# Optimization experiments

Hardware: AMD Instinct MI355X
Metric: run time of the kernel (lower is better)

The kernel has to match this reference:

```python
import jax, jax.numpy as jnp
import numpy as np

EMB_DIM = 512
LATENT_DIM = 64
D = EMB_DIM + LATENT_DIM  # 576, kernel input per side
H1, H2 = 512, 256         # MLPKernel hidden widths
B, N, M = 2, 1024, 256


def setup_inputs() -> dict:
    key = jax.random.key(0)
    ks = jax.random.split(key, 10)
    def w(k, shape, fan_in):
        return (jax.random.normal(k, shape, dtype=jnp.float32) / np.sqrt(fan_in)).astype(jnp.float32)
    return {
        "Phi_A": jax.random.normal(ks[0], (B, N, D), dtype=jnp.float32),
        "Phi_B": jax.random.normal(ks[1], (B, M, D), dtype=jnp.float32),
        # MLPKernel params: layer1 acts on concat([a,b]) (2D -> H1); split into A/B halves
        "W1a": w(ks[2], (D, H1), 2 * D),
        "W1b": w(ks[3], (D, H1), 2 * D),
        "b1": jnp.zeros((H1,), dtype=jnp.float32),
        "W2": w(ks[4], (H1, H2), H1),
        "b2": jnp.zeros((H2,), dtype=jnp.float32),
        "W3": w(ks[5], (H2, 1), H2),
        "b3": jnp.zeros((1,), dtype=jnp.float32),
    }


def reference(Phi_A, Phi_B, W1a, W1b, b1, W2, b2, W3, b3):
    # Pairwise MLP kernel: for every (n, m), MLP(concat(Phi_A[b,n], Phi_B[b,m])).
    # First layer on concat == a@W1a + b@W1b; project each side once, then broadcast-add.
    a_proj = jnp.einsum("bnd,dh->bnh", Phi_A, W1a)          # (B, N, H1)
    b_proj = jnp.einsum("bmd,dh->bmh", Phi_B, W1b)          # (B, M, H1)
    h1 = jax.nn.relu(a_proj[:, :, None, :] + b_proj[:, None, :, :] + b1)  # (B, N, M, H1)
    h2 = jax.nn.relu(jnp.einsum("bnmh,hk->bnmk", h1, W2) + b2)            # (B, N, M, H2)
    dro = jnp.einsum("bnmk,ko->bnmo", h2, W3)[..., 0] + b3[0]             # (B, N, M)
    return dro
```

## Files before the change

kernel.cpp:

```cpp
#include <hip/hip_runtime.h>

typedef float  f4  __attribute__((ext_vector_type(4)));
typedef __bf16 bf8 __attribute__((ext_vector_type(8)));

constexpr int B_ = 2, N_ = 1024, M_ = 256, D_ = 576, H1_ = 512, H2_ = 256;

__device__ __forceinline__ void gload_lds16(const void* g, void* l) {
    __builtin_amdgcn_global_load_lds((const __attribute__((address_space(1))) void*)g,
                                     (__attribute__((address_space(3))) void*)l, 16, 0, 0);
}

__global__ __launch_bounds__(256) void k_prep(
    const float* __restrict__ PhiA, const float* __restrict__ PhiB,
    const float* __restrict__ W1a, const float* __restrict__ W1b, const float* __restrict__ W2,
    __bf16* __restrict__ phiAb, __bf16* __restrict__ phiBb,
    __bf16* __restrict__ w1aT, __bf16* __restrict__ w1bT, __bf16* __restrict__ w2T) {
    __shared__ float tl[32][33];
    int bid = blockIdx.x;
    if (bid < 704) {
        const float* src; __bf16* dst; int R, C, t0;
        if (bid < 288)      { src = W1a; dst = w1aT; R = D_;  C = H1_; t0 = bid; }
        else if (bid < 576) { src = W1b; dst = w1bT; R = D_;  C = H1_; t0 = bid - 288; }
        else                { src = W2;  dst = w2T;  R = H1_; C = H2_; t0 = bid - 576; }
        const int tilesC = C / 32;
        const int r0 = (t0 / tilesC) * 32, c0 = (t0 % tilesC) * 32;
        const int tx = threadIdx.x & 31, ty = threadIdx.x >> 5;
        #pragma unroll
        for (int i = 0; i < 4; ++i)
            tl[ty + i * 8][tx] = src[(size_t)(r0 + ty + i * 8) * C + c0 + tx];
        __syncthreads();
        #pragma unroll
        for (int i = 0; i < 4; ++i)
            dst[(size_t)(c0 + ty + i * 8) * R + r0 + tx] = (__bf16)tl[tx][ty + i * 8];
    } else {
        int i = (bid - 704) * 2048 + threadIdx.x * 8;
        const float* s; __bf16* d;
        if (bid < 1280) { s = PhiA; d = phiAb; }
        else            { s = PhiB; d = phiBb; i -= 1179648; }
        f4 v0 = *(const f4*)(s + i), v1 = *(const f4*)(s + i + 4);
        bf8 o;
        #pragma unroll
        for (int j = 0; j < 4; ++j) { o[j] = (__bf16)v0[j]; o[4 + j] = (__bf16)v1[j]; }
        *(bf8*)(d + i) = o;
    }
}

__global__ __launch_bounds__(256, 2) void k_proj(
    const __bf16* __restrict__ phiAb, const __bf16* __restrict__ phiBb,
    const __bf16* __restrict__ w1aT, const __bf16* __restrict__ w1bT,
    const float* __restrict__ b1, float* __restrict__ aproj, __bf16* __restrict__ bprojh) {
    __shared__ __bf16 as_[2][64 * 64];
    __shared__ __bf16 ws_[2][64 * 64];
    const int t = threadIdx.x, l15 = t & 15, g = (t >> 4) & 3, wid = t >> 6;
    const int wr = wid >> 1, wc = wid & 1;
    const int bx = blockIdx.x, c0 = blockIdx.y * 64;
    const __bf16* src; const __bf16* wt; int rows0; bool isA;
    if (bx < 32) { src = phiAb; wt = w1aT; rows0 = bx * 64;        isA = true; }
    else         { src = phiBb; wt = w1bT; rows0 = (bx - 32) * 64; isA = false; }

#define STG_P(arr, gbase, grow0, kk) do {                                         \
    _Pragma("unroll")                                                             \
    for (int i_ = 0; i_ < 2; ++i_) {                                              \
        int c_ = t + i_ * 256; int row_ = c_ >> 3; int gg_ = (c_ & 7) ^ (row_ & 7);\
        gload_lds16((gbase) + (size_t)((grow0) + row_) * D_ + (kk) + gg_ * 8,     \
                    (char*)(arr) + c_ * 16);                                      \
    } } while (0)

    f4 acc[2][2];
    #pragma unroll
    for (int fr = 0; fr < 2; ++fr)
        #pragma unroll
        for (int cf = 0; cf < 2; ++cf) acc[fr][cf] = (f4)0.0f;

    STG_P(as_[0], src, rows0, 0); STG_P(ws_[0], wt, c0, 0);
    asm volatile("s_waitcnt vmcnt(0)" ::: "memory");
    __builtin_amdgcn_s_barrier();
    STG_P(as_[1], src, rows0, 64); STG_P(ws_[1], wt, c0, 64);

    #pragma unroll 1
    for (int kt = 0; kt < 9; ++kt) {
        const int cur = kt & 1;
        #pragma unroll
        for (int ks = 0; ks < 2; ++ks) {
            bf8 av[2], bv[2];
            #pragma unroll
            for (int fr = 0; fr < 2; ++fr) {
                int row = wr * 32 + fr * 16 + l15;
                av[fr] = *(const bf8*)((const char*)(&as_[cur][0]) +
                         row * 128 + ((ks * 64 + g * 16) ^ ((row & 7) << 4)));
            }
            #pragma unroll
            for (int cf = 0; cf < 2; ++cf) {
                int col = wc * 32 + cf * 16 + l15;
                bv[cf] = *(const bf8*)((const char*)(&ws_[cur][0]) +
                         col * 128 + ((ks * 64 + g * 16) ^ ((col & 7) << 4)));
            }
            #pragma unroll
            for (int fr = 0; fr < 2; ++fr)
                #pragma unroll
                for (int cf = 0; cf < 2; ++cf)
                    acc[fr][cf] = __builtin_amdgcn_mfma_f32_16x16x32_bf16(av[fr], bv[cf], acc[fr][cf], 0, 0, 0);
        }
        if (kt == 8) break;
        asm volatile("s_waitcnt vmcnt(0) lgkmcnt(0)" ::: "memory");
        __builtin_amdgcn_s_barrier();
        if (kt < 7) { STG_P(as_[cur], src, rows0, (kt + 2) * 64); STG_P(ws_[cur], wt, c0, (kt + 2) * 64); }
    }

    #pragma unroll
    for (int fr = 0; fr < 2; ++fr)
        #pragma unroll
        for (int cf = 0; cf < 2; ++cf) {
            int col = c0 + wc * 32 + cf * 16 + l15;
            int row = rows0 + wr * 32 + fr * 16 + g * 4;
            if (isA) {
                float bb = b1[col];
                #pragma unroll
                for (int j = 0; j < 4; ++j)
                    aproj[(size_t)(row + j) * H1_ + col] = acc[fr][cf][j] + bb;
            } else {
                #pragma unroll
                for (int j = 0; j < 4; ++j)
                    bprojh[(size_t)(row + j) * H1_ + col] = (__bf16)acc[fr][cf][j];
            }
        }
#undef STG_P
}

__global__ __launch_bounds__(512, 2) void k_main(
    const float* __restrict__ aproj, const __bf16* __restrict__ bprojh,
    const __bf16* __restrict__ w2T, const float* __restrict__ b2,
    const float* __restrict__ w3, const float* __restrict__ b3,
    float* __restrict__ outp) {
    __shared__ float  apl[16 * 512];
    __shared__ __bf16 bpl[16 * 512];
    __shared__ __bf16 w2l[2][256 * 64];
    __shared__ float  part[2][256];

    const int t = threadIdx.x, l15 = t & 15, g = (t >> 4) & 3, wid = t >> 6;
    const int wr = wid >> 1, wc = wid & 1;
    const int bid = blockIdx.x;
    const int bn0 = (bid >> 4) << 4;
    const int m0 = (bid & 15) << 4;
    const int bprow0 = ((bn0 >> 10) << 8) + m0;

#define STAGE_W2M(buf, kk) do {                                                   \
    _Pragma("unroll")                                                             \
    for (int i_ = 0; i_ < 4; ++i_) {                                              \
        int c_ = t + i_ * 512; int col_ = c_ >> 3; int gg_ = (c_ & 7) ^ (col_ & 7);\
        gload_lds16(w2T + (size_t)col_ * H1_ + (kk) + gg_ * 8,                    \
                    (char*)(&w2l[(buf)][0]) + c_ * 16);                           \
    } } while (0)

#define STAGE_AP() do {                                                           \
    _Pragma("unroll")                                                             \
    for (int i_ = 0; i_ < 4; ++i_) {                                              \
        int c_ = t + i_ * 512;                                                    \
        gload_lds16(aproj + (size_t)(bn0 + (c_ >> 7)) * H1_ + (c_ & 127) * 4,     \
                    (char*)apl + c_ * 16);                                        \
    } } while (0)

#define STAGE_BP() do {                                                           \
    _Pragma("unroll")                                                             \
    for (int i_ = 0; i_ < 2; ++i_) {                                              \
        int c_ = t + i_ * 512; int row_ = c_ >> 6;                                \
        int wb_ = (((c_ & 63) * 16) ^ ((row_ & 7) << 4)) >> 1;                    \
        gload_lds16(bprojh + (size_t)(bprow0 + row_) * H1_ + wb_,                 \
                    (char*)bpl + c_ * 16);                                        \
    } } while (0)

    f4 acc[4][8];
    #pragma unroll
    for (int fr = 0; fr < 4; ++fr)
        #pragma unroll
        for (int cf = 0; cf < 8; ++cf) acc[fr][cf] = (f4)0.0f;

    float b2v[8], w3v[8];
    #pragma unroll
    for (int cf = 0; cf < 8; ++cf) {
        int col = wc * 128 + cf * 16 + l15;
        b2v[cf] = b2[col]; w3v[cf] = w3[col];
    }

    STAGE_AP(); STAGE_BP(); STAGE_W2M(0, 0);
    asm volatile("s_waitcnt vmcnt(0)" ::: "memory");
    __builtin_amdgcn_s_barrier();
    STAGE_W2M(1, 64);

    #pragma unroll 1
    for (int kt = 0; kt < 8; ++kt) {
        const int cur = kt & 1;
        const int kb = kt * 64;
        #pragma unroll
        for (int ks = 0; ks < 2; ++ks) {
            bf8 bpv = *(const bf8*)((const char*)bpl + l15 * 1024 +
                      (((kb + ks * 32 + g * 8) * 2) ^ ((l15 & 7) << 4)));
            float bpf[8];
            #pragma unroll
            for (int j = 0; j < 8; ++j) bpf[j] = (float)bpv[j];
            bf8 bv[8];
            #pragma unroll
            for (int cf = 0; cf < 8; ++cf) {
                int col = wc * 128 + cf * 16 + l15;
                bv[cf] = *(const bf8*)((const char*)(&w2l[cur][0]) +
                         col * 128 + ((ks * 64 + g * 16) ^ ((col & 7) << 4)));
            }
            __builtin_amdgcn_s_setprio(1);
            #pragma unroll
            for (int fr = 0; fr < 4; ++fr) {
                const int n_l = wr * 4 + fr;
                const float* apw = apl + n_l * 512 + kb + ks * 32 + g * 8;
                f4 a0 = *(const f4*)apw, a1 = *(const f4*)(apw + 4);
                bf8 av;
                #pragma unroll
                for (int j = 0; j < 4; ++j) {
                    av[j]     = (__bf16)fmaxf(a0[j] + bpf[j],     0.0f);
                    av[4 + j] = (__bf16)fmaxf(a1[j] + bpf[4 + j], 0.0f);
                }
                #pragma unroll
                for (int cf = 0; cf < 8; ++cf)
                    acc[fr][cf] = __builtin_amdgcn_mfma_f32_16x16x32_bf16(av, bv[cf], acc[fr][cf], 0, 0, 0);
            }
            __builtin_amdgcn_s_setprio(0);
        }
        if (kt == 7) break;
        asm volatile("s_waitcnt vmcnt(0) lgkmcnt(0)" ::: "memory");
        __builtin_amdgcn_s_barrier();
        if (kt < 6) STAGE_W2M(cur, (kt + 2) * 64);
    }

    #pragma unroll
    for (int fr = 0; fr < 4; ++fr) {
        #pragma unroll
        for (int j = 0; j < 4; ++j) {
            float s = 0.0f;
            #pragma unroll
            for (int cf = 0; cf < 8; ++cf)
                s += fmaxf(acc[fr][cf][j] + b2v[cf], 0.0f) * w3v[cf];
            s += __shfl_xor(s, 1); s += __shfl_xor(s, 2);
            s += __shfl_xor(s, 4); s += __shfl_xor(s, 8);
            if (l15 == 0) part[wc][wr * 64 + fr * 16 + g * 4 + j] = s;
        }
    }
    __syncthreads();
    if (t < 256) {
        float o = part[0][t] + part[1][t] + b3[0];
        outp[(size_t)(bn0 + (t >> 4)) * M_ + m0 + (t & 15)] = o;
    }
#undef STAGE_W2M
#undef STAGE_AP
#undef STAGE_BP
}

extern "C" void kernel_launch(void* const* d_in, const int* in_sizes, int n_in,
                              void* d_out, int out_size, void* d_ws, size_t ws_size,
                              hipStream_t stream) {
    (void)in_sizes; (void)n_in; (void)out_size; (void)ws_size;
    const float* PhiA = (const float*)d_in[0];
    const float* PhiB = (const float*)d_in[1];
    const float* W1a  = (const float*)d_in[2];
    const float* W1b  = (const float*)d_in[3];
    const float* b1   = (const float*)d_in[4];
    const float* W2   = (const float*)d_in[5];
    const float* b2   = (const float*)d_in[6];
    const float* W3   = (const float*)d_in[7];
    const float* b3   = (const float*)d_in[8];
    float* out = (float*)d_out;

    char* ws = (char*)d_ws;
    float*  aproj  = (float*)(ws);
    __bf16* bprojh = (__bf16*)(ws + 4194304);
    __bf16* phiAb  = (__bf16*)(ws + 4718592);
    __bf16* phiBb  = (__bf16*)(ws + 7077888);
    __bf16* w1aT   = (__bf16*)(ws + 7667712);
    __bf16* w1bT   = (__bf16*)(ws + 8257536);
    __bf16* w2T    = (__bf16*)(ws + 8847360);

    k_prep<<<1424, 256, 0, stream>>>(PhiA, PhiB, W1a, W1b, W2, phiAb, phiBb, w1aT, w1bT, w2T);
    k_proj<<<dim3(40, 8), 256, 0, stream>>>(phiAb, phiBb, w1aT, w1bT, b1, aproj, bprojh);
    k_main<<<2048, 512, 0, stream>>>(aproj, bprojh, w2T, b2, W3, b3, out);
}
```

Baseline: 236.7 us.

## Fuse Phi bf16 conversion into projection GEMM and restructure main K-loop staging

The bf16 conversion of Phi_A/Phi_B moves out of the prep kernel and into k_proj's A-tile staging, which also grows to 128x128 tiles with 512 threads. The weight transpose uses 64x64 tiles. k_main stages W2 in 32-wide K chunks with a new swizzle, precomputed LDS offsets, a fully unrolled 16-step loop and vmcnt-based prefetch waits. This saves the extra pass that wrote and reread bf16 Phi, but k_proj now issues register-path fp32 loads instead of direct-to-LDS copies, and k_main takes two barriers per K step.

Result: slower. 250.5 us (+5.8%).

```diff
diff --git a/kernel.cpp b/kernel.cpp
--- a/kernel.cpp
+++ b/kernel.cpp
@@ -11,81 +11,84 @@
 }
 
 __global__ __launch_bounds__(256) void k_prep(
+    const float* __restrict__ W1a, const float* __restrict__ W1b, const float* __restrict__ W2,
+    __bf16* __restrict__ w1aT, __bf16* __restrict__ w1bT, __bf16* __restrict__ w2T) {
+    __shared__ float tl[64][65];
+    int bid = blockIdx.x;
+    const float* src; __bf16* dst; int R, C, t0;
+    if (bid < 72)       { src = W1a; dst = w1aT; R = D_;  C = H1_; t0 = bid; }
+    else if (bid < 144) { src = W1b; dst = w1bT; R = D_;  C = H1_; t0 = bid - 72; }
+    else                { src = W2;  dst = w2T;  R = H1_; C = H2_; t0 = bid - 144; }
+    const int tilesC = C / 64;
+    const int r0 = (t0 / tilesC) * 64, c0 = (t0 % tilesC) * 64;
+    const int tx = threadIdx.x & 63, ty = threadIdx.x >> 6;
+    #pragma unroll
+    for (int i = 0; i < 16; ++i)
+        tl[ty + i * 4][tx] = src[(size_t)(r0 + ty + i * 4) * C + c0 + tx];
+    __syncthreads();
+    #pragma unroll
+    for (int i = 0; i < 16; ++i)
+        dst[(size_t)(c0 + ty + i * 4) * R + r0 + tx] = (__bf16)tl[tx][ty + i * 4];
+}
+
+__global__ __launch_bounds__(512, 2) void k_proj(
     const float* __restrict__ PhiA, const float* __restrict__ PhiB,
-    const float* __restrict__ W1a, const float* __restrict__ W1b, const float* __restrict__ W2,
-    __bf16* __restrict__ phiAb, __bf16* __restrict__ phiBb,
-    __bf16* __restrict__ w1aT, __bf16* __restrict__ w1bT, __bf16* __restrict__ w2T) {
-    __shared__ float tl[32][33];
-    int bid = blockIdx.x;
-    if (bid < 704) {
-        const float* src; __bf16* dst; int R, C, t0;
-        if (bid < 288)      { src = W1a; dst = w1aT; R = D_;  C = H1_; t0 = bid; }
-        else if (bid < 576) { src = W1b; dst = w1bT; R = D_;  C = H1_; t0 = bid - 288; }
-        else                { src = W2;  dst = w2T;  R = H1_; C = H2_; t0 = bid - 576; }
-        const int tilesC = C / 32;
-        const int r0 = (t0 / tilesC) * 32, c0 = (t0 % tilesC) * 32;
-        const int tx = threadIdx.x & 31, ty = threadIdx.x >> 5;
-        #pragma unroll
-        for (int i = 0; i < 4; ++i)
-            tl[ty + i * 8][tx] = src[(size_t)(r0 + ty + i * 8) * C + c0 + tx];
-        __syncthreads();
-        #pragma unroll
-        for (int i = 0; i < 4; ++i)
-            dst[(size_t)(c0 + ty + i * 8) * R + r0 + tx] = (__bf16)tl[tx][ty + i * 8];
-    } else {
-        int i = (bid - 704) * 2048 + threadIdx.x * 8;
-        const float* s; __bf16* d;
-        if (bid < 1280) { s = PhiA; d = phiAb; }
-        else            { s = PhiB; d = phiBb; i -= 1179648; }
-        f4 v0 = *(const f4*)(s + i), v1 = *(const f4*)(s + i + 4);
-        bf8 o;
-        #pragma unroll
-        for (int j = 0; j < 4; ++j) { o[j] = (__bf16)v0[j]; o[4 + j] = (__bf16)v1[j]; }
-        *(bf8*)(d + i) = o;
-    }
-}
-
-__global__ __launch_bounds__(256, 2) void k_proj(
-    const __bf16* __restrict__ phiAb, const __bf16* __restrict__ phiBb,
     const __bf16* __restrict__ w1aT, const __bf16* __restrict__ w1bT,
     const float* __restrict__ b1, float* __restrict__ aproj, __bf16* __restrict__ bprojh) {
-    __shared__ __bf16 as_[2][64 * 64];
-    __shared__ __bf16 ws_[2][64 * 64];
+    __shared__ __bf16 as_[2][128 * 64];
+    __shared__ __bf16 ws_[2][128 * 64];
     const int t = threadIdx.x, l15 = t & 15, g = (t >> 4) & 3, wid = t >> 6;
-    const int wr = wid >> 1, wc = wid & 1;
-    const int bx = blockIdx.x, c0 = blockIdx.y * 64;
-    const __bf16* src; const __bf16* wt; int rows0; bool isA;
-    if (bx < 32) { src = phiAb; wt = w1aT; rows0 = bx * 64;        isA = true; }
-    else         { src = phiBb; wt = w1bT; rows0 = (bx - 32) * 64; isA = false; }
-
-#define STG_P(arr, gbase, grow0, kk) do {                                         \
+    const int wr = wid >> 2, wc = wid & 3;
+    const int by = blockIdx.x, c0 = blockIdx.y * 128;
+    const bool isA = (by < 16);
+    const float* srcf = isA ? PhiA : PhiB;
+    const int rows0 = isA ? by * 128 : (by - 16) * 128;
+    const __bf16* wt = isA ? w1aT : w1bT;
+
+    const int ra = t >> 2, kc = (t & 3) * 16;
+
+#define STG_A(buf, kk) do {                                                       \
+    const float* ap_ = srcf + (size_t)(rows0 + ra) * D_ + (kk) + kc;              \
+    f4 v0_ = *(const f4*)ap_, v1_ = *(const f4*)(ap_ + 4),                        \
+       v2_ = *(const f4*)(ap_ + 8), v3_ = *(const f4*)(ap_ + 12);                 \
+    bf8 h0_, h1_;                                                                 \
+    _Pragma("unroll")                                                             \
+    for (int j_ = 0; j_ < 4; ++j_) {                                              \
+        h0_[j_] = (__bf16)v0_[j_]; h0_[4 + j_] = (__bf16)v1_[j_];                 \
+        h1_[j_] = (__bf16)v2_[j_]; h1_[4 + j_] = (__bf16)v3_[j_];                 \
+    }                                                                             \
+    *(bf8*)((char*)(&as_[(buf)][0]) + ra * 128 + ((kc * 2) ^ ((ra & 7) << 4)))      = h0_; \
+    *(bf8*)((char*)(&as_[(buf)][0]) + ra * 128 + ((kc * 2 + 16) ^ ((ra & 7) << 4))) = h1_; \
+    } while (0)
+
+#define STG_W(buf, kk) do {                                                       \
     _Pragma("unroll")                                                             \
     for (int i_ = 0; i_ < 2; ++i_) {                                              \
-        int c_ = t + i_ * 256; int row_ = c_ >> 3; int gg_ = (c_ & 7) ^ (row_ & 7);\
-        gload_lds16((gbase) + (size_t)((grow0) + row_) * D_ + (kk) + gg_ * 8,     \
-                    (char*)(arr) + c_ * 16);                                      \
-    } } while (0)
-
-    f4 acc[2][2];
-    #pragma unroll
-    for (int fr = 0; fr < 2; ++fr)
+        int c_ = t + i_ * 512; int col_ = c_ >> 3; int gg_ = (c_ & 7) ^ (col_ & 7);\
+        gload_lds16(wt + (size_t)(c0 + col_) * D_ + (kk) + gg_ * 8,               \
+                    (char*)(&ws_[(buf)][0]) + c_ * 16);                           \
+    } } while (0)
+
+    f4 acc[4][2];
+    #pragma unroll
+    for (int fr = 0; fr < 4; ++fr)
         #pragma unroll
         for (int cf = 0; cf < 2; ++cf) acc[fr][cf] = (f4)0.0f;
 
-    STG_P(as_[0], src, rows0, 0); STG_P(ws_[0], wt, c0, 0);
-    asm volatile("s_waitcnt vmcnt(0)" ::: "memory");
+    STG_A(0, 0); STG_W(0, 0);
+    asm volatile("s_waitcnt vmcnt(0) lgkmcnt(0)" ::: "memory");
     __builtin_amdgcn_s_barrier();
-    STG_P(as_[1], src, rows0, 64); STG_P(ws_[1], wt, c0, 64);
+    STG_A(1, 64); STG_W(1, 64);
 
     #pragma unroll 1
     for (int kt = 0; kt < 9; ++kt) {
         const int cur = kt & 1;
         #pragma unroll
         for (int ks = 0; ks < 2; ++ks) {
-            bf8 av[2], bv[2];
-            #pragma unroll
-            for (int fr = 0; fr < 2; ++fr) {
-                int row = wr * 32 + fr * 16 + l15;
+            bf8 av[4], bv[2];
+            #pragma unroll
+            for (int fr = 0; fr < 4; ++fr) {
+                int row = wr * 64 + fr * 16 + l15;
                 av[fr] = *(const bf8*)((const char*)(&as_[cur][0]) +
                          row * 128 + ((ks * 64 + g * 16) ^ ((row & 7) << 4)));
             }
@@ -96,7 +99,7 @@
                          col * 128 + ((ks * 64 + g * 16) ^ ((col & 7) << 4)));
             }
             #pragma unroll
-            for (int fr = 0; fr < 2; ++fr)
+            for (int fr = 0; fr < 4; ++fr)
                 #pragma unroll
                 for (int cf = 0; cf < 2; ++cf)
                     acc[fr][cf] = __builtin_amdgcn_mfma_f32_16x16x32_bf16(av[fr], bv[cf], acc[fr][cf], 0, 0, 0);
@@ -104,15 +107,15 @@
         if (kt == 8) break;
         asm volatile("s_waitcnt vmcnt(0) lgkmcnt(0)" ::: "memory");
         __builtin_amdgcn_s_barrier();
-        if (kt < 7) { STG_P(as_[cur], src, rows0, (kt + 2) * 64); STG_P(ws_[cur], wt, c0, (kt + 2) * 64); }
-    }
-
-    #pragma unroll
-    for (int fr = 0; fr < 2; ++fr)
+        if (kt < 7) { STG_A(cur, (kt + 2) * 64); STG_W(cur, (kt + 2) * 64); }
+    }
+
+    #pragma unroll
+    for (int fr = 0; fr < 4; ++fr)
         #pragma unroll
         for (int cf = 0; cf < 2; ++cf) {
             int col = c0 + wc * 32 + cf * 16 + l15;
-            int row = rows0 + wr * 32 + fr * 16 + g * 4;
+            int row = rows0 + wr * 64 + fr * 16 + g * 4;
             if (isA) {
                 float bb = b1[col];
                 #pragma unroll
@@ -124,7 +127,8 @@
                     bprojh[(size_t)(row + j) * H1_ + col] = (__bf16)acc[fr][cf][j];
             }
         }
-#undef STG_P
+#undef STG_A
+#undef STG_W
 }
 
 __global__ __launch_bounds__(512, 2) void k_main(
@@ -134,7 +138,7 @@
     float* __restrict__ outp) {
     __shared__ float  apl[16 * 512];
     __shared__ __bf16 bpl[16 * 512];
-    __shared__ __bf16 w2l[2][256 * 64];
+    __shared__ __bf16 w2l[2][256 * 32];
     __shared__ float  part[2][256];
 
     const int t = threadIdx.x, l15 = t & 15, g = (t >> 4) & 3, wid = t >> 6;
@@ -144,12 +148,25 @@
     const int m0 = (bid & 15) << 4;
     const int bprow0 = ((bn0 >> 10) << 8) + m0;
 
-#define STAGE_W2M(buf, kk) do {                                                   \
-    _Pragma("unroll")                                                             \
-    for (int i_ = 0; i_ < 4; ++i_) {                                              \
-        int c_ = t + i_ * 512; int col_ = c_ >> 3; int gg_ = (c_ & 7) ^ (col_ & 7);\
-        gload_lds16(w2T + (size_t)col_ * H1_ + (kk) + gg_ * 8,                    \
-                    (char*)(&w2l[(buf)][0]) + c_ * 16);                           \
+    int offA[4];
+    #pragma unroll
+    for (int fr = 0; fr < 4; ++fr) offA[fr] = (wr * 4 + fr) * 2048 + g * 32;
+    int offB[8];
+    #pragma unroll
+    for (int cf = 0; cf < 8; ++cf) {
+        int col = wc * 128 + cf * 16 + l15;
+        int cp = col >> 1, sp = (((col & 1) << 2) + g) ^ (cp & 7);
+        offB[cf] = cp * 128 + sp * 16;
+    }
+    const int offP = l15 * 1024 + (((g ^ (l15 & 3)) | (l15 & 4)) << 4);
+
+#define STAGE_W2M(buf, ktn) do {                                                  \
+    _Pragma("unroll")                                                             \
+    for (int i_ = 0; i_ < 2; ++i_) {                                              \
+        int c_ = t + i_ * 512; int cp_ = c_ >> 3; int sp_ = c_ & 7;               \
+        int si_ = sp_ ^ (cp_ & 7); int col_ = cp_ * 2 + (si_ >> 2);               \
+        gload_lds16(w2T + (size_t)col_ * H1_ + (ktn) * 32 + (si_ & 3) * 8,        \
+                    (char*)w2l + (buf) * 16384 + c_ * 16);                        \
     } } while (0)
 
 #define STAGE_AP() do {                                                           \
@@ -163,9 +180,8 @@
 #define STAGE_BP() do {                                                           \
     _Pragma("unroll")                                                             \
     for (int i_ = 0; i_ < 2; ++i_) {                                              \
-        int c_ = t + i_ * 512; int row_ = c_ >> 6;                                \
-        int wb_ = (((c_ & 63) * 16) ^ ((row_ & 7) << 4)) >> 1;                    \
-        gload_lds16(bprojh + (size_t)(bprow0 + row_) * H1_ + wb_,                 \
+        int c_ = t + i_ * 512; int row_ = c_ >> 6; int kc_ = (c_ & 63) ^ (row_ & 7);\
+        gload_lds16(bprojh + (size_t)(bprow0 + row_) * H1_ + kc_ * 8,             \
                     (char*)bpl + c_ * 16);                                        \
     } } while (0)
 
@@ -182,51 +198,49 @@
         b2v[cf] = b2[col]; w3v[cf] = w3[col];
     }
 
-    STAGE_AP(); STAGE_BP(); STAGE_W2M(0, 0);
-    asm volatile("s_waitcnt vmcnt(0)" ::: "memory");
+    STAGE_AP(); STAGE_BP(); STAGE_W2M(0, 0); STAGE_W2M(1, 1);
+    asm volatile("s_waitcnt vmcnt(2)" ::: "memory");
     __builtin_amdgcn_s_barrier();
-    STAGE_W2M(1, 64);
-
-    #pragma unroll 1
-    for (int kt = 0; kt < 8; ++kt) {
+
+    #pragma unroll
+    for (int kt = 0; kt < 16; ++kt) {
         const int cur = kt & 1;
-        const int kb = kt * 64;
-        #pragma unroll
-        for (int ks = 0; ks < 2; ++ks) {
-            bf8 bpv = *(const bf8*)((const char*)bpl + l15 * 1024 +
-                      (((kb + ks * 32 + g * 8) * 2) ^ ((l15 & 7) << 4)));
-            float bpf[8];
-            #pragma unroll
-            for (int j = 0; j < 8; ++j) bpf[j] = (float)bpv[j];
-            bf8 bv[8];
-            #pragma unroll
-            for (int cf = 0; cf < 8; ++cf) {
-                int col = wc * 128 + cf * 16 + l15;
-                bv[cf] = *(const bf8*)((const char*)(&w2l[cur][0]) +
-                         col * 128 + ((ks * 64 + g * 16) ^ ((col & 7) << 4)));
-            }
-            __builtin_amdgcn_s_setprio(1);
-            #pragma unroll
-            for (int fr = 0; fr < 4; ++fr) {
-                const int n_l = wr * 4 + fr;
-                const float* apw = apl + n_l * 512 + kb + ks * 32 + g * 8;
-                f4 a0 = *(const f4*)apw, a1 = *(const f4*)(apw + 4);
-                bf8 av;
-                #pragma unroll
-                for (int j = 0; j < 4; ++j) {
-                    av[j]     = (__bf16)fmaxf(a0[j] + bpf[j],     0.0f);
-                    av[4 + j] = (__bf16)fmaxf(a1[j] + bpf[4 + j], 0.0f);
-                }
-                #pragma unroll
-                for (int cf = 0; cf < 8; ++cf)
-                    acc[fr][cf] = __builtin_amdgcn_mfma_f32_16x16x32_bf16(av, bv[cf], acc[fr][cf], 0, 0, 0);
-            }
-            __builtin_amdgcn_s_setprio(0);
-        }
-        if (kt == 7) break;
-        asm volatile("s_waitcnt vmcnt(0) lgkmcnt(0)" ::: "memory");
-        __builtin_amdgcn_s_barrier();
-        if (kt < 6) STAGE_W2M(cur, (kt + 2) * 64);
+        bf8 bpv = *(const bf8*)((const char*)bpl + (offP ^ (kt * 64)));
+        bf8 bv[8];
+        #pragma unroll
+        for (int cf = 0; cf < 8; ++cf)
+            bv[cf] = *(const bf8*)((const char*)w2l + offB[cf] + cur * 16384);
+        f4 a0[4], a1[4];
+        #pragma unroll
+        for (int fr = 0; fr < 4; ++fr) {
+            a0[fr] = *(const f4*)((const char*)apl + offA[fr] + kt * 128);
+            a1[fr] = *(const f4*)((const char*)apl + offA[fr] + kt * 128 + 16);
+        }
+        float bpf[8];
+        #pragma unroll
+        for (int j = 0; j < 8; ++j) bpf[j] = (float)bpv[j];
+        __builtin_amdgcn_s_setprio(1);
+        #pragma unroll
+        for (int fr = 0; fr < 4; ++fr) {
+            bf8 av;
+            #pragma unroll
+            for (int j = 0; j < 4; ++j) {
+                av[j]     = (__bf16)fmaxf(a0[fr][j] + bpf[j],     0.0f);
+                av[4 + j] = (__bf16)fmaxf(a1[fr][j] + bpf[4 + j], 0.0f);
+            }
+            #pragma unroll
+            for (int cf = 0; cf < 8; ++cf)
+                acc[fr][cf] = __builtin_amdgcn_mfma_f32_16x16x32_bf16(av, bv[cf], acc[fr][cf], 0, 0, 0);
+        }
+        __builtin_amdgcn_s_setprio(0);
+        if (kt < 15) {
+            asm volatile("" ::: "memory");
+            __builtin_amdgcn_s_barrier();
+            if (kt < 14) STAGE_W2M(cur, kt + 2);
+            if (kt < 14) asm volatile("s_waitcnt vmcnt(2)" ::: "memory");
+            else         asm volatile("s_waitcnt vmcnt(0)" ::: "memory");
+            __builtin_amdgcn_s_barrier();
+        }
     }
 
     #pragma unroll
@@ -270,13 +284,11 @@
     char* ws = (char*)d_ws;
     float*  aproj  = (float*)(ws);
     __bf16* bprojh = (__bf16*)(ws + 4194304);
-    __bf16* phiAb  = (__bf16*)(ws + 4718592);
-    __bf16* phiBb  = (__bf16*)(ws + 7077888);
-    __bf16* w1aT   = (__bf16*)(ws + 7667712);
-    __bf16* w1bT   = (__bf16*)(ws + 8257536);
-    __bf16* w2T    = (__bf16*)(ws + 8847360);
-
-    k_prep<<<1424, 256, 0, stream>>>(PhiA, PhiB, W1a, W1b, W2, phiAb, phiBb, w1aT, w1bT, w2T);
-    k_proj<<<dim3(40, 8), 256, 0, stream>>>(phiAb, phiBb, w1aT, w1bT, b1, aproj, bprojh);
+    __bf16* w1aT   = (__bf16*)(ws + 4718592);
+    __bf16* w1bT   = (__bf16*)(ws + 5308416);
+    __bf16* w2T    = (__bf16*)(ws + 5898240);
+
+    k_prep<<<176, 256, 0, stream>>>(W1a, W1b, W2, w1aT, w1bT, w2T);
+    k_proj<<<dim3(20, 4), 512, 0, stream>>>(PhiA, PhiB, w1aT, w1bT, b1, aproj, bprojh);
     k_main<<<2048, 512, 0, stream>>>(aproj, bprojh, w2T, b2, W3, b3, out);
 }
```
